# Kernel tuning notes

Hardware: AMD Instinct MI355X
Metric: run time of the kernel (lower is better)

Reference implementation:

```python
import jax, jax.numpy as jnp
import numpy as np

N = 50000      # nodes
DIM = 128      # feature dim
H = 4          # heads
C = DIM // H   # per-head channels
E = 800000     # edges (before self-loops)
LRELU_SLOPE = 0.2
LN_EPS = 1e-5


def setup_inputs() -> dict:
    key = jax.random.key(0)
    ks = jax.random.split(key, 12)
    def p(k, shape, scale=0.05):
        return jax.random.normal(k, shape, jnp.float32) * scale
    return {
        "x": jax.random.normal(ks[0], (N, DIM), jnp.float32),
        "edge_index": jax.random.randint(ks[1], (2, E), 0, N),
        "W1": p(ks[2], (DIM, DIM)), "b1": jnp.zeros((DIM,), jnp.float32),
        "att_src1": p(ks[3], (H, C)), "att_dst1": p(ks[4], (H, C)),
        "W2": p(ks[5], (DIM, DIM)), "b2": jnp.zeros((DIM,), jnp.float32),
        "att_src2": p(ks[6], (H, C)), "att_dst2": p(ks[7], (H, C)),
        "gate_W": p(ks[8], (2 * DIM, 2)), "gate_b": jnp.zeros((2,), jnp.float32),
        "ln_gamma": jnp.ones((DIM,), jnp.float32), "ln_beta": jnp.zeros((DIM,), jnp.float32),
    }


def _gat(x, src, dst, W, b, a_src, a_dst):
    # Linear transform, split heads: [N, H, C]
    h = (x @ W).reshape(-1, H, C)
    # Per-node attention logits per head: [N, H]
    e_src = jnp.einsum("nhc,hc->nh", h, a_src)
    e_dst = jnp.einsum("nhc,hc->nh", h, a_dst)
    # Per-edge logits (edge j->i: src=j, dst=i): [E, H]
    e = jax.nn.leaky_relu(e_src[src] + e_dst[dst], LRELU_SLOPE)
    # Segment softmax over edges sharing a destination (self-loops guarantee >=1 edge/node)
    m = jax.ops.segment_max(e, dst, num_segments=N)
    p = jnp.exp(e - m[dst])
    s = jax.ops.segment_sum(p, dst, num_segments=N)
    alpha = p / s[dst]                                   # [E, H]
    # Weighted scatter-add aggregation
    out = jax.ops.segment_sum(h[src] * alpha[..., None], dst, num_segments=N)
    return out.reshape(-1, H * C) + b                    # [N, DIM]


def reference(x, edge_index, W1, b1, att_src1, att_dst1, W2, b2, att_src2, att_dst2,
              gate_W, gate_b, ln_gamma, ln_beta):
    n = x.shape[0]
    loops = jnp.arange(n, dtype=edge_index.dtype)
    src = jnp.concatenate([edge_index[0], loops])  # PyG GATConv add_self_loops=True
    dst = jnp.concatenate([edge_index[1], loops])
    out1 = _gat(x, src, dst, W1, b1, att_src1, att_dst1)
    out2 = _gat(x, src, dst, W2, b2, att_src2, att_dst2)
    gate = jax.nn.softmax(jnp.concatenate([out1, out2], axis=-1) @ gate_W + gate_b, axis=-1)
    out = gate[:, 0:1] * out1 + gate[:, 1:2] * out2
    # residual + LayerNorm (dropout is identity in eval)
    y = x + out
    mu = jnp.mean(y, axis=-1, keepdims=True)
    var = jnp.var(y, axis=-1, keepdims=True)
    return (y - mu) * jax.lax.rsqrt(var + LN_EPS) * ln_gamma + ln_beta
```

## Files before the change

kernel.cpp:

```cpp
#include <hip/hip_runtime.h>
#include <hip/hip_bf16.h>


typedef unsigned short u16;
typedef __bf16 bf16x8 __attribute__((ext_vector_type(8)));
typedef float f32x4 __attribute__((ext_vector_type(4)));

#define LRELU_SLOPE 0.2f
#define LN_EPS 1e-5f
#define SH 8

__device__ __forceinline__ float bfbits(unsigned int hi_bits) {
    union { unsigned int i; float f; } v; v.i = hi_bits; return v.f;
}
__device__ __forceinline__ float bflo(unsigned int u) { return bfbits(u << 16); }
__device__ __forceinline__ float bfhi(unsigned int u) { return bfbits(u & 0xFFFF0000u); }
__device__ __forceinline__ u16 f2bf(float f) {
    union { float f; unsigned int i; } v; v.f = f;
    unsigned int lsb = (v.i >> 16) & 1u;
    v.i += 0x7FFFu + lsb;
    return (u16)(v.i >> 16);
}

__global__ void k_prep(const float* __restrict__ W1, const float* __restrict__ W2,
                       u16* __restrict__ wb, int* __restrict__ deg8, int n) {
    int i = blockIdx.x * 256 + threadIdx.x;
    if (i < 32768) {
        int col = i >> 7, k = i & 127;
        float v = (col < 128) ? W1[k * 128 + col] : W2[k * 128 + (col - 128)];
        wb[i] = f2bf(v);
    }
    if (i < n) {
#pragma unroll
        for (int x = 0; x < SH; x++) deg8[x * n + i] = 0;
    }
}

__global__ __launch_bounds__(256) void k_cg(const float* __restrict__ x,
                                            const u16* __restrict__ wb,
                                            unsigned int* __restrict__ hbp, int n,
                                            const int* __restrict__ ei,
                                            int* __restrict__ deg8, int E, int Gg) {
    if ((int)blockIdx.x >= Gg) {
        int i = ((int)blockIdx.x - Gg) * 256 + threadIdx.x;
        if (i < E) {
            int sh = (i >> 8) & (SH - 1);
            atomicAdd(&deg8[sh * n + ei[E + i]], 1);
        }
        return;
    }
    int wave = threadIdx.x >> 6, lane = threadIdx.x & 63;
    int quad = lane >> 4, r16 = lane & 15;
    int row = blockIdx.x * 64 + wave * 16 + r16;
    int arow = (row < n) ? row : n - 1;
    const float* xp = x + (size_t)arow * 128 + quad * 8;
    union { u16 u[8]; bf16x8 b; } ar;
    bf16x8 a[4];
#pragma unroll
    for (int ks = 0; ks < 4; ks++) {
        float4 lo = *(const float4*)(xp + ks * 32);
        float4 hi = *(const float4*)(xp + ks * 32 + 4);
        ar.u[0] = f2bf(lo.x); ar.u[1] = f2bf(lo.y); ar.u[2] = f2bf(lo.z); ar.u[3] = f2bf(lo.w);
        ar.u[4] = f2bf(hi.x); ar.u[5] = f2bf(hi.y); ar.u[6] = f2bf(hi.z); ar.u[7] = f2bf(hi.w);
        a[ks] = ar.b;
    }
    f32x4 acc[16];
#pragma unroll
    for (int t = 0; t < 16; t++) acc[t] = (f32x4){0.f, 0.f, 0.f, 0.f};
    const u16* bbase = wb + r16 * 128 + quad * 8;
#pragma unroll
    for (int t = 0; t < 16; t++) {
        const u16* bp = bbase + t * 2048;
#pragma unroll
        for (int ks = 0; ks < 4; ks++) {
            bf16x8 b = *(const bf16x8*)(bp + ks * 32);
            acc[t] = __builtin_amdgcn_mfma_f32_16x16x32_bf16(a[ks], b, acc[t], 0, 0, 0);
        }
    }
    int row0 = blockIdx.x * 64 + wave * 16 + quad * 4;
#pragma unroll
    for (int t = 0; t < 8; t++) {
        int c = t * 16 + r16;
#pragma unroll
        for (int g = 0; g < 4; g++) {
            int gr = row0 + g;
            if (gr < n) {
                unsigned int pv = ((unsigned int)f2bf(acc[t + 8][g]) << 16) | f2bf(acc[t][g]);
                hbp[(size_t)gr * 128 + c] = pv;
            }
        }
    }
}

__global__ void k_lb(const unsigned int* __restrict__ hbp,
                     const float* __restrict__ as1, const float* __restrict__ ad1,
                     const float* __restrict__ as2, const float* __restrict__ ad2,
                     float* __restrict__ es, float* __restrict__ ed, int n,
                     const int* __restrict__ deg8, int* __restrict__ bsum, int Gl) {
    __shared__ int s[256];
    if ((int)blockIdx.x >= Gl) {
        int bid = (int)blockIdx.x - Gl;
        int i = bid * 256 + threadIdx.x;
        int v = 0;
        if (i < n) {
#pragma unroll
            for (int x = 0; x < SH; x++) v += deg8[x * n + i];
        }
        s[threadIdx.x] = v;
        __syncthreads();
        for (int o = 128; o; o >>= 1) {
            if (threadIdx.x < o) s[threadIdx.x] += s[threadIdx.x + o];
            __syncthreads();
        }
        if (threadIdx.x == 0) bsum[bid] = s[0];
        return;
    }
    int i = blockIdx.x * 256 + threadIdx.x;
    if (i >= n * 4) return;
    int node = i >> 2, head = i & 3;
    const uint4* hv = (const uint4*)(hbp + (size_t)node * 128 + head * 32);
    const float* a1 = as1 + head * 32;
    const float* d1 = ad1 + head * 32;
    const float* a2 = as2 + head * 32;
    const float* d2 = ad2 + head * 32;
    float s1 = 0.f, t1 = 0.f, s2 = 0.f, t2 = 0.f;
#pragma unroll
    for (int q = 0; q < 8; q++) {
        uint4 w = hv[q];
        unsigned int ws[4] = {w.x, w.y, w.z, w.w};
#pragma unroll
        for (int h = 0; h < 4; h++) {
            int c = q * 4 + h;
            float v1 = bflo(ws[h]), v2 = bfhi(ws[h]);
            s1 += v1 * a1[c]; t1 += v1 * d1[c];
            s2 += v2 * a2[c]; t2 += v2 * d2[c];
        }
    }
    es[node * 8 + head]     = s1;
    ed[node * 8 + head]     = t1;
    es[node * 8 + 4 + head] = s2;
    ed[node * 8 + 4 + head] = t2;
}

__global__ void k_scan(int* __restrict__ deg8, const int* __restrict__ bsum,
                       int* __restrict__ offs, int nb, int n) {
    __shared__ int s[256];
    __shared__ int bp;
    int t = threadIdx.x;
    int bv = (t < nb) ? bsum[t] : 0;
    s[t] = bv;
    __syncthreads();
    for (int o = 1; o < 256; o <<= 1) {
        int u = (t >= o) ? s[t - o] : 0;
        __syncthreads();
        s[t] += u;
        __syncthreads();
    }
    if (t == (int)blockIdx.x) bp = s[t] - bv;
    __syncthreads();
    int i = blockIdx.x * 256 + t;
    int d[SH];
    int v = 0;
    if (i < n) {
#pragma unroll
        for (int x = 0; x < SH; x++) { d[x] = deg8[x * n + i]; v += d[x]; }
    }
    s[t] = v;
    __syncthreads();
    for (int o = 1; o < 256; o <<= 1) {
        int u = (t >= o) ? s[t - o] : 0;
        __syncthreads();
        s[t] += u;
        __syncthreads();
    }
    if (i < n) {
        int e = bp + s[t] - v;
        offs[i] = e;
        int run = e;
#pragma unroll
        for (int x = 0; x < SH; x++) { deg8[x * n + i] = run; run += d[x]; }
        if (i == n - 1) offs[n] = e + v;
    }
}

__global__ void k_fill(const int* __restrict__ ei, int* __restrict__ cursor8,
                       const float* __restrict__ es, const float* __restrict__ ed,
                       int* __restrict__ ssrc, uint4* __restrict__ w, int E, int n) {
    int i = blockIdx.x * 256 + threadIdx.x;
    if (i >= E) return;
    int s = ei[i], d = ei[E + i];
    int sh = (i >> 8) & (SH - 1);
    int pos = atomicAdd(&cursor8[sh * n + d], 1);
    ssrc[pos] = s;
    float4 eslo = *(const float4*)(es + s * 8);
    float4 eshi = *(const float4*)(es + s * 8 + 4);
    float4 edlo = *(const float4*)(ed + d * 8);
    float4 edhi = *(const float4*)(ed + d * 8 + 4);
    float e1[4] = {eslo.x + edlo.x, eslo.y + edlo.y, eslo.z + edlo.z, eslo.w + edlo.w};
    float e2[4] = {eshi.x + edhi.x, eshi.y + edhi.y, eshi.z + edhi.z, eshi.w + edhi.w};
    unsigned int uw[4];
#pragma unroll
    for (int h = 0; h < 4; h++) {
        float a = e1[h]; a = (a > 0.f) ? a : LRELU_SLOPE * a;
        float b = e2[h]; b = (b > 0.f) ? b : LRELU_SLOPE * b;
        uw[h] = ((unsigned int)f2bf(__expf(b)) << 16) | f2bf(__expf(a));
    }
    w[pos] = make_uint4(uw[0], uw[1], uw[2], uw[3]);
}

__device__ __forceinline__ float wred(float v) {
#pragma unroll
    for (int off = 32; off; off >>= 1) v += __shfl_xor(v, off, 64);
    return v;
}

__device__ __forceinline__ unsigned int hsel(uint4 w, int head) {
    unsigned int r = (head == 0) ? w.x : (head == 1) ? w.y : (head == 2) ? w.z : w.w;
    return r;
}

__global__ __launch_bounds__(256) void k_agg(
    const int* __restrict__ offs, const int* __restrict__ ssrc,
    const unsigned int* __restrict__ hbp, const uint4* __restrict__ w4,
    const float* __restrict__ es, const float* __restrict__ ed,
    const float* __restrict__ b1, const float* __restrict__ b2,
    const float* __restrict__ gW, const float* __restrict__ gb,
    const float* __restrict__ x, const float* __restrict__ gamma,
    const float* __restrict__ beta, float* __restrict__ out, int n) {
    int wave = threadIdx.x >> 6, lane = threadIdx.x & 63;
    int node = blockIdx.x * 4 + wave;
    if (node >= n) return;
    node = __builtin_amdgcn_readfirstlane(node);

    int ca = lane * 2, cb = ca + 1;
    int head = lane >> 4;

    const float* esp = es + node * 8;
    const float* edp = ed + node * 8;
    float e1s = esp[head] + edp[head];
    float e2s = esp[4 + head] + edp[4 + head];
    e1s = (e1s > 0.f) ? e1s : LRELU_SLOPE * e1s;
    e2s = (e2s > 0.f) ? e2s : LRELU_SLOPE * e2s;
    float w1s = __expf(e1s), w2s = __expf(e2s);
    uint2 qs = *(const uint2*)(hbp + (size_t)node * 128 + ca);
    float l1 = w1s, l2 = w2s;
    float a1a = w1s * bflo(qs.x), a1b = w1s * bflo(qs.y);
    float a2a = w2s * bfhi(qs.x), a2b = w2s * bfhi(qs.y);

    int beg = offs[node], end = offs[node + 1];
    int k = beg;
#define ACC(wp, q) { \
        float ww1 = bflo(wp), ww2 = bfhi(wp); \
        l1 += ww1; l2 += ww2; \
        a1a += ww1 * bflo(q.x); a1b += ww1 * bflo(q.y); \
        a2a += ww2 * bfhi(q.x); a2b += ww2 * bfhi(q.y); }
    for (; k + 3 < end; k += 4) {
        int j0 = ssrc[k], j1 = ssrc[k + 1], j2 = ssrc[k + 2], j3 = ssrc[k + 3];
        uint4 w0 = w4[k], w1v = w4[k + 1], w2v = w4[k + 2], w3v = w4[k + 3];
        uint2 q0 = *(const uint2*)(hbp + (size_t)j0 * 128 + ca);
        uint2 q1 = *(const uint2*)(hbp + (size_t)j1 * 128 + ca);
        uint2 q2 = *(const uint2*)(hbp + (size_t)j2 * 128 + ca);
        uint2 q3 = *(const uint2*)(hbp + (size_t)j3 * 128 + ca);
        unsigned int wp0 = hsel(w0, head), wp1 = hsel(w1v, head);
        unsigned int wp2 = hsel(w2v, head), wp3 = hsel(w3v, head);
        ACC(wp0, q0) ACC(wp1, q1) ACC(wp2, q2) ACC(wp3, q3)
    }
    for (; k < end; k++) {
        int j = ssrc[k];
        uint4 wv = w4[k];
        uint2 q = *(const uint2*)(hbp + (size_t)j * 128 + ca);
        unsigned int wp = hsel(wv, head);
        ACC(wp, q)
    }
#undef ACC

    float2 b1v = *(const float2*)(b1 + ca);
    float2 b2v = *(const float2*)(b2 + ca);
    float r1 = 1.f / l1, r2 = 1.f / l2;
    float o1a = a1a * r1 + b1v.x;
    float o1b = a1b * r1 + b1v.y;
    float o2a = a2a * r2 + b2v.x;
    float o2b = a2b * r2 + b2v.y;

    float2 g1a = *(const float2*)(gW + 2 * ca);
    float2 g1b = *(const float2*)(gW + 2 * cb);
    float2 g2a = *(const float2*)(gW + 2 * (128 + ca));
    float2 g2b = *(const float2*)(gW + 2 * (128 + cb));
    float p0 = o1a * g1a.x + o1b * g1b.x + o2a * g2a.x + o2b * g2b.x;
    float p1 = o1a * g1a.y + o1b * g1b.y + o2a * g2a.y + o2b * g2b.y;
    p0 = wred(p0) + gb[0];
    p1 = wred(p1) + gb[1];
    float mg = fmaxf(p0, p1);
    float eg0 = __expf(p0 - mg), eg1 = __expf(p1 - mg);
    float g0 = eg0 / (eg0 + eg1), g1 = 1.f - g0;

    float2 xv = *(const float2*)(x + (size_t)node * 128 + ca);
    float ya = xv.x + g0 * o1a + g1 * o2a;
    float yb = xv.y + g0 * o1b + g1 * o2b;

    float s  = wred(ya + yb);
    float ss = wred(ya * ya + yb * yb);
    float mean = s * (1.f / 128.f);
    float var  = ss * (1.f / 128.f) - mean * mean;
    float rstd = rsqrtf(var + LN_EPS);
    float2 gv = *(const float2*)(gamma + ca);
    float2 bv = *(const float2*)(beta + ca);
    float2 ov;
    ov.x = (ya - mean) * rstd * gv.x + bv.x;
    ov.y = (yb - mean) * rstd * gv.y + bv.y;
    *(float2*)(out + (size_t)node * 128 + ca) = ov;
}

extern "C" void kernel_launch(void* const* d_in, const int* in_sizes, int n_in,
                              void* d_out, int out_size, void* d_ws, size_t ws_size,
                              hipStream_t stream) {
    const float* x   = (const float*)d_in[0];
    const int*   ei  = (const int*)d_in[1];
    const float* W1  = (const float*)d_in[2];
    const float* b1  = (const float*)d_in[3];
    const float* as1 = (const float*)d_in[4];
    const float* ad1 = (const float*)d_in[5];
    const float* W2  = (const float*)d_in[6];
    const float* b2  = (const float*)d_in[7];
    const float* as2 = (const float*)d_in[8];
    const float* ad2 = (const float*)d_in[9];
    const float* gW  = (const float*)d_in[10];
    const float* gb  = (const float*)d_in[11];
    const float* gamma = (const float*)d_in[12];
    const float* beta  = (const float*)d_in[13];
    float* out = (float*)d_out;

    int n = in_sizes[0] / 128;
    int E = in_sizes[1] / 2;

    char* p = (char*)d_ws;
    auto take = [&](size_t bytes) {
        char* q = p;
        p += (bytes + 255) & ~(size_t)255;
        return (void*)q;
    };
    u16* wb    = (u16*)take((size_t)256 * 128 * 2);
    unsigned int* hbp = (unsigned int*)take((size_t)n * 128 * 4);
    float* es  = (float*)take((size_t)n * 8 * 4);
    float* ed  = (float*)take((size_t)n * 8 * 4);
    int* deg8  = (int*)take((size_t)SH * n * 4);
    int* offs  = (int*)take((size_t)(n + 1) * 4);
    int* bsum  = (int*)take((size_t)256 * 4);
    int* ssrc  = (int*)take((size_t)E * 4);
    uint4* w   = (uint4*)take((size_t)E * 16);

    int nb = (n + 255) / 256;
    int Gg = (n + 63) / 64;
    int Gc = (E + 255) / 256;
    int Gl = (n * 4 + 255) / 256;

    k_prep<<<nb, 256, 0, stream>>>(W1, W2, wb, deg8, n);
    k_cg<<<Gg + Gc, 256, 0, stream>>>(x, wb, hbp, n, ei, deg8, E, Gg);
    k_lb<<<Gl + nb, 256, 0, stream>>>(hbp, as1, ad1, as2, ad2, es, ed, n,
                                      deg8, bsum, Gl);
    k_scan<<<nb, 256, 0, stream>>>(deg8, bsum, offs, nb, n);
    k_fill<<<Gc, 256, 0, stream>>>(ei, deg8, es, ed, ssrc, w, E, n);
    k_agg<<<(n + 3) / 4, 256, 0, stream>>>(offs, ssrc, hbp, w, es, ed,
                                           b1, b2, gW, gb, x, gamma, beta, out, n);
}
```

Baseline: 269.7 us.

## Compute edge attention weights on the fly in aggregation instead of materializing them

The per-edge bf16 exp-weight array (16 bytes per edge) is no longer written in the fill kernel and read back in aggregation. Instead, aggregation gathers the per-source logits as a float2 per head and computes leaky-relu plus exp inline. The node-logit computation moves out of the bsum kernel and is merged into the fill launch as extra blocks, with es/ed relaid out as interleaved [head][layer] pairs. This removes a large write/read stream but adds a random gather and exp work per edge in the aggregation loop.

```diff
diff --git a/kernel.cpp b/kernel.cpp
--- a/kernel.cpp
+++ b/kernel.cpp
@@ -92,54 +92,21 @@
     }
 }
 
-__global__ void k_lb(const unsigned int* __restrict__ hbp,
-                     const float* __restrict__ as1, const float* __restrict__ ad1,
-                     const float* __restrict__ as2, const float* __restrict__ ad2,
-                     float* __restrict__ es, float* __restrict__ ed, int n,
-                     const int* __restrict__ deg8, int* __restrict__ bsum, int Gl) {
+__global__ void k_sb(const int* __restrict__ deg8, int* __restrict__ bsum, int n) {
     __shared__ int s[256];
-    if ((int)blockIdx.x >= Gl) {
-        int bid = (int)blockIdx.x - Gl;
-        int i = bid * 256 + threadIdx.x;
-        int v = 0;
-        if (i < n) {
-#pragma unroll
-            for (int x = 0; x < SH; x++) v += deg8[x * n + i];
-        }
-        s[threadIdx.x] = v;
-        __syncthreads();
-        for (int o = 128; o; o >>= 1) {
-            if (threadIdx.x < o) s[threadIdx.x] += s[threadIdx.x + o];
-            __syncthreads();
-        }
-        if (threadIdx.x == 0) bsum[bid] = s[0];
-        return;
-    }
     int i = blockIdx.x * 256 + threadIdx.x;
-    if (i >= n * 4) return;
-    int node = i >> 2, head = i & 3;
-    const uint4* hv = (const uint4*)(hbp + (size_t)node * 128 + head * 32);
-    const float* a1 = as1 + head * 32;
-    const float* d1 = ad1 + head * 32;
-    const float* a2 = as2 + head * 32;
-    const float* d2 = ad2 + head * 32;
-    float s1 = 0.f, t1 = 0.f, s2 = 0.f, t2 = 0.f;
-#pragma unroll
-    for (int q = 0; q < 8; q++) {
-        uint4 w = hv[q];
-        unsigned int ws[4] = {w.x, w.y, w.z, w.w};
-#pragma unroll
-        for (int h = 0; h < 4; h++) {
-            int c = q * 4 + h;
-            float v1 = bflo(ws[h]), v2 = bfhi(ws[h]);
-            s1 += v1 * a1[c]; t1 += v1 * d1[c];
-            s2 += v2 * a2[c]; t2 += v2 * d2[c];
-        }
-    }
-    es[node * 8 + head]     = s1;
-    ed[node * 8 + head]     = t1;
-    es[node * 8 + 4 + head] = s2;
-    ed[node * 8 + 4 + head] = t2;
+    int v = 0;
+    if (i < n) {
+#pragma unroll
+        for (int x = 0; x < SH; x++) v += deg8[x * n + i];
+    }
+    s[threadIdx.x] = v;
+    __syncthreads();
+    for (int o = 128; o; o >>= 1) {
+        if (threadIdx.x < o) s[threadIdx.x] += s[threadIdx.x + o];
+        __syncthreads();
+    }
+    if (threadIdx.x == 0) bsum[blockIdx.x] = s[0];
 }
 
 __global__ void k_scan(int* __restrict__ deg8, const int* __restrict__ bsum,
@@ -183,29 +150,44 @@
     }
 }
 
-__global__ void k_fill(const int* __restrict__ ei, int* __restrict__ cursor8,
-                       const float* __restrict__ es, const float* __restrict__ ed,
-                       int* __restrict__ ssrc, uint4* __restrict__ w, int E, int n) {
+__global__ void k_fl(const int* __restrict__ ei, int* __restrict__ cursor8,
+                     int* __restrict__ ssrc, int E, int n,
+                     const unsigned int* __restrict__ hbp,
+                     const float* __restrict__ as1, const float* __restrict__ ad1,
+                     const float* __restrict__ as2, const float* __restrict__ ad2,
+                     float* __restrict__ es, float* __restrict__ ed, int Gc) {
+    if ((int)blockIdx.x >= Gc) {
+        int i = ((int)blockIdx.x - Gc) * 256 + threadIdx.x;
+        if (i >= n * 4) return;
+        int node = i >> 2, head = i & 3;
+        const uint4* hv = (const uint4*)(hbp + (size_t)node * 128 + head * 32);
+        const float* a1 = as1 + head * 32;
+        const float* d1 = ad1 + head * 32;
+        const float* a2 = as2 + head * 32;
+        const float* d2 = ad2 + head * 32;
+        float s1 = 0.f, t1 = 0.f, s2 = 0.f, t2 = 0.f;
+#pragma unroll
+        for (int q = 0; q < 8; q++) {
+            uint4 w = hv[q];
+            unsigned int ws[4] = {w.x, w.y, w.z, w.w};
+#pragma unroll
+            for (int h = 0; h < 4; h++) {
+                int c = q * 4 + h;
+                float v1 = bflo(ws[h]), v2 = bfhi(ws[h]);
+                s1 += v1 * a1[c]; t1 += v1 * d1[c];
+                s2 += v2 * a2[c]; t2 += v2 * d2[c];
+            }
+        }
+        *(float2*)(es + node * 8 + head * 2) = make_float2(s1, s2);
+        *(float2*)(ed + node * 8 + head * 2) = make_float2(t1, t2);
+        return;
+    }
     int i = blockIdx.x * 256 + threadIdx.x;
     if (i >= E) return;
     int s = ei[i], d = ei[E + i];
     int sh = (i >> 8) & (SH - 1);
     int pos = atomicAdd(&cursor8[sh * n + d], 1);
     ssrc[pos] = s;
-    float4 eslo = *(const float4*)(es + s * 8);
-    float4 eshi = *(const float4*)(es + s * 8 + 4);
-    float4 edlo = *(const float4*)(ed + d * 8);
-    float4 edhi = *(const float4*)(ed + d * 8 + 4);
-    float e1[4] = {eslo.x + edlo.x, eslo.y + edlo.y, eslo.z + edlo.z, eslo.w + edlo.w};
-    float e2[4] = {eshi.x + edhi.x, eshi.y + edhi.y, eshi.z + edhi.z, eshi.w + edhi.w};
-    unsigned int uw[4];
-#pragma unroll
-    for (int h = 0; h < 4; h++) {
-        float a = e1[h]; a = (a > 0.f) ? a : LRELU_SLOPE * a;
-        float b = e2[h]; b = (b > 0.f) ? b : LRELU_SLOPE * b;
-        uw[h] = ((unsigned int)f2bf(__expf(b)) << 16) | f2bf(__expf(a));
-    }
-    w[pos] = make_uint4(uw[0], uw[1], uw[2], uw[3]);
 }
 
 __device__ __forceinline__ float wred(float v) {
@@ -214,14 +196,9 @@
     return v;
 }
 
-__device__ __forceinline__ unsigned int hsel(uint4 w, int head) {
-    unsigned int r = (head == 0) ? w.x : (head == 1) ? w.y : (head == 2) ? w.z : w.w;
-    return r;
-}
-
 __global__ __launch_bounds__(256) void k_agg(
     const int* __restrict__ offs, const int* __restrict__ ssrc,
-    const unsigned int* __restrict__ hbp, const uint4* __restrict__ w4,
+    const unsigned int* __restrict__ hbp,
     const float* __restrict__ es, const float* __restrict__ ed,
     const float* __restrict__ b1, const float* __restrict__ b2,
     const float* __restrict__ gW, const float* __restrict__ gb,
@@ -232,47 +209,51 @@
     if (node >= n) return;
     node = __builtin_amdgcn_readfirstlane(node);
 
-    int ca = lane * 2, cb = ca + 1;
+    int ca = lane * 2;
     int head = lane >> 4;
-
-    const float* esp = es + node * 8;
-    const float* edp = ed + node * 8;
-    float e1s = esp[head] + edp[head];
-    float e2s = esp[4 + head] + edp[4 + head];
-    e1s = (e1s > 0.f) ? e1s : LRELU_SLOPE * e1s;
-    e2s = (e2s > 0.f) ? e2s : LRELU_SLOPE * e2s;
-    float w1s = __expf(e1s), w2s = __expf(e2s);
-    uint2 qs = *(const uint2*)(hbp + (size_t)node * 128 + ca);
-    float l1 = w1s, l2 = w2s;
-    float a1a = w1s * bflo(qs.x), a1b = w1s * bflo(qs.y);
-    float a2a = w2s * bfhi(qs.x), a2b = w2s * bfhi(qs.y);
-
-    int beg = offs[node], end = offs[node + 1];
-    int k = beg;
-#define ACC(wp, q) { \
-        float ww1 = bflo(wp), ww2 = bfhi(wp); \
+    int hh = head * 2;
+
+    float2 edv = *(const float2*)(ed + node * 8 + hh);
+    float ed1 = edv.x, ed2 = edv.y;
+
+    float l1 = 0.f, l2 = 0.f;
+    float a1a = 0.f, a1b = 0.f, a2a = 0.f, a2b = 0.f;
+
+#define EDGE(sv, q) { \
+        float e1 = sv.x + ed1; e1 = fmaxf(e1, LRELU_SLOPE * e1); \
+        float e2 = sv.y + ed2; e2 = fmaxf(e2, LRELU_SLOPE * e2); \
+        float ww1 = __expf(e1), ww2 = __expf(e2); \
         l1 += ww1; l2 += ww2; \
         a1a += ww1 * bflo(q.x); a1b += ww1 * bflo(q.y); \
         a2a += ww2 * bfhi(q.x); a2b += ww2 * bfhi(q.y); }
+
+    {
+        float2 svs = *(const float2*)(es + node * 8 + hh);
+        uint2 qs = *(const uint2*)(hbp + (size_t)node * 128 + ca);
+        EDGE(svs, qs)
+    }
+
+    int beg = offs[node], end = offs[node + 1];
+    int k = beg;
     for (; k + 3 < end; k += 4) {
         int j0 = ssrc[k], j1 = ssrc[k + 1], j2 = ssrc[k + 2], j3 = ssrc[k + 3];
-        uint4 w0 = w4[k], w1v = w4[k + 1], w2v = w4[k + 2], w3v = w4[k + 3];
+        float2 s0 = *(const float2*)(es + j0 * 8 + hh);
+        float2 s1 = *(const float2*)(es + j1 * 8 + hh);
+        float2 s2 = *(const float2*)(es + j2 * 8 + hh);
+        float2 s3 = *(const float2*)(es + j3 * 8 + hh);
         uint2 q0 = *(const uint2*)(hbp + (size_t)j0 * 128 + ca);
         uint2 q1 = *(const uint2*)(hbp + (size_t)j1 * 128 + ca);
         uint2 q2 = *(const uint2*)(hbp + (size_t)j2 * 128 + ca);
         uint2 q3 = *(const uint2*)(hbp + (size_t)j3 * 128 + ca);
-        unsigned int wp0 = hsel(w0, head), wp1 = hsel(w1v, head);
-        unsigned int wp2 = hsel(w2v, head), wp3 = hsel(w3v, head);
-        ACC(wp0, q0) ACC(wp1, q1) ACC(wp2, q2) ACC(wp3, q3)
+        EDGE(s0, q0) EDGE(s1, q1) EDGE(s2, q2) EDGE(s3, q3)
     }
     for (; k < end; k++) {
         int j = ssrc[k];
-        uint4 wv = w4[k];
+        float2 sv = *(const float2*)(es + j * 8 + hh);
         uint2 q = *(const uint2*)(hbp + (size_t)j * 128 + ca);
-        unsigned int wp = hsel(wv, head);
-        ACC(wp, q)
-    }
-#undef ACC
+        EDGE(sv, q)
+    }
+#undef EDGE
 
     float2 b1v = *(const float2*)(b1 + ca);
     float2 b2v = *(const float2*)(b2 + ca);
@@ -282,6 +263,7 @@
     float o2a = a2a * r2 + b2v.x;
     float o2b = a2b * r2 + b2v.y;
 
+    int cb = ca + 1;
     float2 g1a = *(const float2*)(gW + 2 * ca);
     float2 g1b = *(const float2*)(gW + 2 * cb);
     float2 g2a = *(const float2*)(gW + 2 * (128 + ca));
@@ -347,7 +329,6 @@
     int* offs  = (int*)take((size_t)(n + 1) * 4);
     int* bsum  = (int*)take((size_t)256 * 4);
     int* ssrc  = (int*)take((size_t)E * 4);
-    uint4* w   = (uint4*)take((size_t)E * 16);
 
     int nb = (n + 255) / 256;
     int Gg = (n + 63) / 64;
@@ -356,10 +337,10 @@
 
     k_prep<<<nb, 256, 0, stream>>>(W1, W2, wb, deg8, n);
     k_cg<<<Gg + Gc, 256, 0, stream>>>(x, wb, hbp, n, ei, deg8, E, Gg);
-    k_lb<<<Gl + nb, 256, 0, stream>>>(hbp, as1, ad1, as2, ad2, es, ed, n,
-                                      deg8, bsum, Gl);
+    k_sb<<<nb, 256, 0, stream>>>(deg8, bsum, n);
     k_scan<<<nb, 256, 0, stream>>>(deg8, bsum, offs, nb, n);
-    k_fill<<<Gc, 256, 0, stream>>>(ei, deg8, es, ed, ssrc, w, E, n);
-    k_agg<<<(n + 3) / 4, 256, 0, stream>>>(offs, ssrc, hbp, w, es, ed,
+    k_fl<<<Gc + Gl, 256, 0, stream>>>(ei, deg8, ssrc, E, n, hbp,
+                                      as1, ad1, as2, ad2, es, ed, Gc);
+    k_agg<<<(n + 3) / 4, 256, 0, stream>>>(offs, ssrc, hbp, es, ed,
                                            b1, b2, gW, gb, x, gamma, beta, out, n);
 }
```

Result: slower. 295.9 us (+9.7%).
